# Performance work log

Measured on AMD Instinct MI355X. Metric: run time of the kernel, lower is better.

Reference implementation:

```python
import jax, jax.numpy as jnp
import numpy as np

HIDDEN_DIM = 64
MEMORY_SLOTS = 4
SEQ_LEN = 24
VOCAB_SIZE = 64
B = 65536


def setup_inputs() -> dict:
    key = jax.random.key(0)
    ks = jax.random.split(key, 16)
    s = 0.05
    inp = {
        "seqs": jax.random.randint(ks[0], (B, SEQ_LEN), 0, VOCAB_SIZE + 2),
        "query_tok": jax.random.randint(ks[1], (B,), 0, VOCAB_SIZE + 2),
        # embedding table [VOCAB+2, H]
        "embed": jax.random.normal(ks[2], (VOCAB_SIZE + 2, HIDDEN_DIM), jnp.float32) * s,
        # joint_net: Linear(H + S*H -> H), ReLU, Linear(H -> H), ReLU  (weights stored [in, out])
        "W1": jax.random.normal(ks[3], (HIDDEN_DIM + MEMORY_SLOTS * HIDDEN_DIM, HIDDEN_DIM), jnp.float32) * s,
        "b1": jax.random.normal(ks[4], (HIDDEN_DIM,), jnp.float32) * s,
        "W2": jax.random.normal(ks[5], (HIDDEN_DIM, HIDDEN_DIM), jnp.float32) * s,
        "b2": jax.random.normal(ks[6], (HIDDEN_DIM,), jnp.float32) * s,
        # write_head: Linear(H -> H)
        "Ww": jax.random.normal(ks[7], (HIDDEN_DIM, HIDDEN_DIM), jnp.float32) * s,
        "bw": jax.random.normal(ks[8], (HIDDEN_DIM,), jnp.float32) * s,
        # evict_head: Linear(H -> MEMORY_SLOTS)
        "We": jax.random.normal(ks[9], (HIDDEN_DIM, MEMORY_SLOTS), jnp.float32) * s,
        "be": jax.random.normal(ks[10], (MEMORY_SLOTS,), jnp.float32) * s,
        # read_head: Linear(2H -> H), ReLU, Linear(H -> VOCAB)
        "Wr1": jax.random.normal(ks[11], (2 * HIDDEN_DIM, HIDDEN_DIM), jnp.float32) * s,
        "br1": jax.random.normal(ks[12], (HIDDEN_DIM,), jnp.float32) * s,
        "Wr2": jax.random.normal(ks[13], (HIDDEN_DIM, VOCAB_SIZE), jnp.float32) * s,
        "br2": jax.random.normal(ks[14], (VOCAB_SIZE,), jnp.float32) * s,
    }
    return inp


def reference(seqs, query_tok, embed, W1, b1, W2, b2, Ww, bw, We, be, Wr1, br1, Wr2, br2):
    # Token embeddings for the first SEQ_LEN-1 positions, scanned over time: [T, B, H]
    emb_seq = jnp.swapaxes(embed[seqs[:, : SEQ_LEN - 1]], 0, 1)

    def step(mem, emb_t):  # mem: [B, S, H], emb_t: [B, H]
        joint_in = jnp.concatenate([emb_t, mem.reshape(mem.shape[0], -1)], axis=-1)  # [B, H + S*H]
        h = jax.nn.relu(joint_in @ W1 + b1)
        h = jax.nn.relu(h @ W2 + b2)                      # [B, H]
        write_vec = h @ Ww + bw                           # [B, H]
        evict_logits = h @ We + be                        # [B, S]
        evict_idx = jnp.argmax(evict_logits, axis=-1)     # [B] hard, non-diff
        mask = jax.nn.one_hot(evict_idx, MEMORY_SLOTS, dtype=bool)[..., None]  # [B, S, 1]
        new_mem = jnp.where(mask, write_vec[:, None, :], mem)
        return new_mem, None

    mem0 = jnp.zeros((seqs.shape[0], MEMORY_SLOTS, HIDDEN_DIM), jnp.float32)
    mem, _ = jax.lax.scan(step, mem0, emb_seq)

    mem_summary = mem.mean(axis=1)                        # [B, H]
    q_emb = embed[query_tok]                              # [B, H]
    r = jnp.concatenate([q_emb, mem_summary], axis=-1)    # [B, 2H]
    logits = jax.nn.relu(r @ Wr1 + br1) @ Wr2 + br2       # [B, VOCAB]
    return logits
```

## Files before the change

kernel.cpp:

```cpp
#include <hip/hip_runtime.h>

#define H       64
#define NSLOT   4
#define NSTEP   23
#define NB      65536
#define NV      66
#define SEQL    24
#define LPE     8
#define TPB     512
#define EPB     128
#define ACTSTR  68
#define MROW    68
#define JL      48
#define MSSTR   (JL * MROW + 4)

#define OFF_EW1   0
#define OFF_EWR1  (NV * H)
#define OFF_M     (2 * NV * H)
#define OFF_PB    (OFF_M + NSLOT * H * H)
#define OFF_HL    (OFF_PB + NSLOT * H)

__global__ __launch_bounds__(256) void k_setup_tables(
    const float* __restrict__ embed, const float* __restrict__ W1, const float* __restrict__ b1,
    const float* __restrict__ Wr1, const float* __restrict__ br1, float* __restrict__ ws)
{
    int idx = blockIdx.x * 256 + threadIdx.x;
    if (idx >= NV * H) return;
    int t = idx >> 6, k = idx & 63;
    float a1 = b1[k], a2 = br1[k];
    for (int j = 0; j < H; ++j) {
        float e = embed[t * H + j];
        a1 = fmaf(e, W1[j * H + k], a1);
        a2 = fmaf(e, Wr1[j * H + k], a2);
    }
    ws[OFF_EW1 + idx]  = a1;
    ws[OFF_EWR1 + idx] = a2;
}

__global__ __launch_bounds__(256) void k_setup_fuse(
    const float* __restrict__ W1, const float* __restrict__ Ww, const float* __restrict__ bw,
    float* __restrict__ ws)
{
    int idx = blockIdx.x * 256 + threadIdx.x;
    if (idx < NSLOT * H * H) {
        int s = idx >> 12, j = (idx >> 6) & 63, k = idx & 63;
        const float* w1s = W1 + (size_t)(H + s * H) * H;
        float acc = 0.f;
        for (int p = 0; p < H; ++p)
            acc = fmaf(Ww[j * H + p], w1s[p * H + k], acc);
        ws[OFF_M + idx] = acc;
    } else if (idx < NSLOT * H * H + NSLOT * H) {
        int r = idx - NSLOT * H * H;
        int s = r >> 6, k = r & 63;
        const float* w1s = W1 + (size_t)(H + s * H) * H;
        float acc = 0.f;
        for (int p = 0; p < H; ++p)
            acc = fmaf(bw[p], w1s[p * H + k], acc);
        ws[OFF_PB + r] = acc;
    }
}

#define FMA8V(w0, w1, a, ACC) do {                                          \
    ACC[0]=fmaf((a),w0.x,ACC[0]); ACC[1]=fmaf((a),w0.y,ACC[1]);            \
    ACC[2]=fmaf((a),w0.z,ACC[2]); ACC[3]=fmaf((a),w0.w,ACC[3]);            \
    ACC[4]=fmaf((a),w1.x,ACC[4]); ACC[5]=fmaf((a),w1.y,ACC[5]);            \
    ACC[6]=fmaf((a),w1.z,ACC[6]); ACC[7]=fmaf((a),w1.w,ACC[7]);            \
} while (0)

#define LOAD8(ptr, A) do {                                                  \
    const float4* _b = (const float4*)(ptr);                                \
    float4 _b0 = _b[0], _b1 = _b[1];                                        \
    A[0]=_b0.x; A[1]=_b0.y; A[2]=_b0.z; A[3]=_b0.w;                        \
    A[4]=_b1.x; A[5]=_b1.y; A[6]=_b1.z; A[7]=_b1.w;                        \
} while (0)

#define STORE8(rowptr, A) do {                                              \
    float4* _d = (float4*)(rowptr);                                         \
    _d[0] = make_float4(A[0], A[1], A[2], A[3]);                            \
    _d[1] = make_float4(A[4], A[5], A[6], A[7]);                            \
} while (0)

__global__ __launch_bounds__(TPB, 1) void k_main(
    const float* __restrict__ W2, const float* __restrict__ b2,
    const float* __restrict__ Ww, const float* __restrict__ bw,
    const float* __restrict__ We, const float* __restrict__ be,
    const float* __restrict__ Wr1, const float* __restrict__ Wr2, const float* __restrict__ br2,
    const int* __restrict__ qtok, const int* __restrict__ seqs,
    const float* __restrict__ ws, float* hl, float* __restrict__ out)
{
    __shared__ float sM[NSLOT * MSSTR];
    __shared__ float sAct[EPB * ACTSTR];
    __shared__ float sPb[NSLOT * 68];
    __shared__ float sWeS[8 * 36];

    const int tid  = threadIdx.x;
    const int m    = tid & (LPE - 1);
    const int g    = tid >> 3;
    const int eA   = g;
    const int eB   = g + 64;
    const int gidA = blockIdx.x * EPB + eA;
    const int gidB = blockIdx.x * EPB + eB;
    const int k0   = m * 8;

    if (tid < 256) {
        int s = tid >> 6, j = tid & 63;
        if (j < JL) {
            const float4* src = (const float4*)(ws + OFF_M + (size_t)(s * H + j) * H);
            float4* dst = (float4*)(sM + s * MSSTR + j * MROW);
#pragma unroll
            for (int k = 0; k < 16; ++k) dst[k] = src[k];
        }
    }
    if (tid >= 256 && tid < 512) {
        int r = tid - 256;
        int s = r >> 6, k = r & 63;
        sPb[s * 68 + k] = ws[OFF_PB + s * H + k];
    }
    if (tid < 256) {
        int mm = tid >> 5, rem = tid & 31;
        sWeS[mm * 36 + rem] = We[tid];
    }
    __syncthreads();

    const float* embW1b  = ws + OFF_EW1;
    const float* embWr1b = ws + OFF_EWR1;
    const float* Mg      = ws + OFF_M;
    float* hlA = hl + (size_t)gidA * (NSLOT * H) + k0;
    float* hlB = hl + (size_t)gidB * (NSLOT * H) + k0;

    float pA0[8], pA1[8], pA2[8], pA3[8], cA[8];
    float pB0[8], pB1[8], pB2[8], pB3[8], cB[8];
#pragma unroll
    for (int i = 0; i < 8; ++i) {
        pA0[i]=0.f; pA1[i]=0.f; pA2[i]=0.f; pA3[i]=0.f; cA[i]=0.f;
        pB0[i]=0.f; pB1[i]=0.f; pB2[i]=0.f; pB3[i]=0.f; cB[i]=0.f;
    }
    int maskA = 0, maskB = 0;

    float b2r[8];
    LOAD8(b2 + k0, b2r);
    const float4 be4 = *(const float4*)be;

    int tokA = seqs[gidA * SEQL];
    int tokB = seqs[gidB * SEQL];

    float accA[8], accB[8];
    float* rowA = sAct + eA * ACTSTR;
    float* rowB = sAct + eB * ACTSTR;

#pragma unroll 1
    for (int t = 0; t < NSTEP; ++t) {
        int tokAn = seqs[gidA * SEQL + t + 1];
        int tokBn = seqs[gidB * SEQL + t + 1];

        {
            float hA[8], hB[8];
            LOAD8(embW1b + tokA * H + k0, hA);
            LOAD8(embW1b + tokB * H + k0, hB);
#pragma unroll
            for (int i = 0; i < 8; ++i) {
                hA[i] = fmaxf(hA[i] + cA[i], 0.f);
                hB[i] = fmaxf(hB[i] + cB[i], 0.f);
            }
            STORE8(rowA + k0, hA);
            STORE8(rowB + k0, hB);
        }

#pragma unroll
        for (int i = 0; i < 8; ++i) { accA[i] = b2r[i]; accB[i] = b2r[i]; }
#pragma unroll 4
        for (int jq = 0; jq < 16; ++jq) {
            float4 a4 = *(const float4*)(rowA + jq * 4);
            float4 b4 = *(const float4*)(rowB + jq * 4);
            float aAv[4] = {a4.x, a4.y, a4.z, a4.w};
            float aBv[4] = {b4.x, b4.y, b4.z, b4.w};
#pragma unroll
            for (int jj = 0; jj < 4; ++jj) {
                const float4* w = (const float4*)(W2 + (jq * 4 + jj) * H + k0);
                float4 w0 = w[0], w1 = w[1];
                FMA8V(w0, w1, aAv[jj], accA);
                FMA8V(w0, w1, aBv[jj], accB);
            }
        }
        float h2A[8], h2B[8];
#pragma unroll
        for (int i = 0; i < 8; ++i) {
            h2A[i] = fmaxf(accA[i], 0.f);
            h2B[i] = fmaxf(accB[i], 0.f);
        }
        STORE8(rowA + k0, h2A);
        STORE8(rowB + k0, h2B);

        float lA0 = 0.f, lA1 = 0.f, lA2 = 0.f, lA3 = 0.f;
        float lB0 = 0.f, lB1 = 0.f, lB2 = 0.f, lB3 = 0.f;
        {
            const float* wsl = sWeS + m * 36;
#pragma unroll
            for (int i = 0; i < 8; ++i) {
                float4 we4 = *(const float4*)(wsl + i * 4);
                lA0 = fmaf(h2A[i], we4.x, lA0); lA1 = fmaf(h2A[i], we4.y, lA1);
                lA2 = fmaf(h2A[i], we4.z, lA2); lA3 = fmaf(h2A[i], we4.w, lA3);
                lB0 = fmaf(h2B[i], we4.x, lB0); lB1 = fmaf(h2B[i], we4.y, lB1);
                lB2 = fmaf(h2B[i], we4.z, lB2); lB3 = fmaf(h2B[i], we4.w, lB3);
            }
        }
#pragma unroll
        for (int d = 1; d <= 4; d <<= 1) {
            lA0 += __shfl_xor(lA0, d); lA1 += __shfl_xor(lA1, d);
            lA2 += __shfl_xor(lA2, d); lA3 += __shfl_xor(lA3, d);
            lB0 += __shfl_xor(lB0, d); lB1 += __shfl_xor(lB1, d);
            lB2 += __shfl_xor(lB2, d); lB3 += __shfl_xor(lB3, d);
        }
        lA0 += be4.x; lA1 += be4.y; lA2 += be4.z; lA3 += be4.w;
        lB0 += be4.x; lB1 += be4.y; lB2 += be4.z; lB3 += be4.w;

        int eSA = 0; float bstA = lA0;
        if (lA1 > bstA) { bstA = lA1; eSA = 1; }
        if (lA2 > bstA) { bstA = lA2; eSA = 2; }
        if (lA3 > bstA) { bstA = lA3; eSA = 3; }
        int eSB = 0; float bstB = lB0;
        if (lB1 > bstB) { bstB = lB1; eSB = 1; }
        if (lB2 > bstB) { bstB = lB2; eSB = 2; }
        if (lB3 > bstB) { bstB = lB3; eSB = 3; }

        bool a0 = (eSA == 0), a1 = (eSA == 1), a2 = (eSA == 2), a3 = (eSA == 3);
        bool b0 = (eSB == 0), b1 = (eSB == 1), b2_ = (eSB == 2), b3 = (eSB == 3);

        STORE8(hlA + eSA * H, h2A);
        STORE8(hlB + eSB * H, h2B);
        maskA |= (1 << eSA);
        maskB |= (1 << eSB);

        LOAD8(sPb + eSA * 68 + k0, accA);
        LOAD8(sPb + eSB * 68 + k0, accB);
        const float* lMA = sM + eSA * MSSTR + k0;
        const float* lMB = sM + eSB * MSSTR + k0;
#pragma unroll 4
        for (int jq = 0; jq < JL / 4; ++jq) {
            float4 a4 = *(const float4*)(rowA + jq * 4);
            float4 b4 = *(const float4*)(rowB + jq * 4);
            float dAv[4] = {a4.x, a4.y, a4.z, a4.w};
            float dBv[4] = {b4.x, b4.y, b4.z, b4.w};
#pragma unroll
            for (int jj = 0; jj < 4; ++jj) {
                int j = jq * 4 + jj;
                const float4* wa = (const float4*)(lMA + j * MROW);
                const float4* wb = (const float4*)(lMB + j * MROW);
                float4 wa0 = wa[0], wa1 = wa[1];
                float4 wb0 = wb[0], wb1 = wb[1];
                FMA8V(wa0, wa1, dAv[jj], accA);
                FMA8V(wb0, wb1, dBv[jj], accB);
            }
        }
        {
            const float* gMA = Mg + (size_t)(eSA * H + JL) * H + k0;
            const float* gMB = Mg + (size_t)(eSB * H + JL) * H + k0;
#pragma unroll 2
            for (int jq = JL / 4; jq < 16; ++jq) {
                float4 a4 = *(const float4*)(rowA + jq * 4);
                float4 b4 = *(const float4*)(rowB + jq * 4);
                float dAv[4] = {a4.x, a4.y, a4.z, a4.w};
                float dBv[4] = {b4.x, b4.y, b4.z, b4.w};
#pragma unroll
                for (int jj = 0; jj < 4; ++jj) {
                    int jr = (jq * 4 + jj) - JL;
                    const float4* wa = (const float4*)(gMA + jr * H);
                    const float4* wb = (const float4*)(gMB + jr * H);
                    float4 wa0 = wa[0], wa1 = wa[1];
                    float4 wb0 = wb[0], wb1 = wb[1];
                    FMA8V(wa0, wa1, dAv[jj], accA);
                    FMA8V(wb0, wb1, dBv[jj], accB);
                }
            }
        }

#pragma unroll
        for (int i = 0; i < 8; ++i) {
            float pvA = accA[i], pvB = accB[i];
            float oldA = a0 ? pA0[i] : a1 ? pA1[i] : a2 ? pA2[i] : pA3[i];
            float oldB = b0 ? pB0[i] : b1 ? pB1[i] : b2_ ? pB2[i] : pB3[i];
            cA[i] += pvA - oldA;
            cB[i] += pvB - oldB;
            pA0[i] = a0 ? pvA : pA0[i];  pA1[i] = a1 ? pvA : pA1[i];
            pA2[i] = a2 ? pvA : pA2[i];  pA3[i] = a3 ? pvA : pA3[i];
            pB0[i] = b0 ? pvB : pB0[i];  pB1[i] = b1 ? pvB : pB1[i];
            pB2[i] = b2_ ? pvB : pB2[i]; pB3[i] = b3 ? pvB : pB3[i];
        }

        tokA = tokAn; tokB = tokBn;
    }

    __threadfence();
    {
        float hsA[8] = {0,0,0,0,0,0,0,0}, hsB[8] = {0,0,0,0,0,0,0,0};
#pragma unroll
        for (int s = 0; s < NSLOT; ++s) {
            float vA[8], vB[8];
            LOAD8(hlA + s * H, vA);
            LOAD8(hlB + s * H, vB);
            float fA = ((maskA >> s) & 1) ? 1.f : 0.f;
            float fB = ((maskB >> s) & 1) ? 1.f : 0.f;
#pragma unroll
            for (int i = 0; i < 8; ++i) {
                hsA[i] = fmaf(fA, vA[i], hsA[i]);
                hsB[i] = fmaf(fB, vB[i], hsB[i]);
            }
        }
        STORE8(rowA + k0, hsA);
        STORE8(rowB + k0, hsB);
    }

    {
        float bwr[8];
        LOAD8(bw + k0, bwr);
        float cntA = (float)__popc(maskA), cntB = (float)__popc(maskB);
#pragma unroll
        for (int i = 0; i < 8; ++i) { accA[i] = cntA * bwr[i]; accB[i] = cntB * bwr[i]; }
    }
#pragma unroll 4
    for (int jq = 0; jq < 16; ++jq) {
        float4 a4 = *(const float4*)(rowA + jq * 4);
        float4 b4 = *(const float4*)(rowB + jq * 4);
        float aAv[4] = {a4.x, a4.y, a4.z, a4.w};
        float aBv[4] = {b4.x, b4.y, b4.z, b4.w};
#pragma unroll
        for (int jj = 0; jj < 4; ++jj) {
            const float4* w = (const float4*)(Ww + (jq * 4 + jj) * H + k0);
            float4 w0 = w[0], w1 = w[1];
            FMA8V(w0, w1, aAv[jj], accA);
            FMA8V(w0, w1, aBv[jj], accB);
        }
    }
    {
        float msA[8], msB[8];
#pragma unroll
        for (int i = 0; i < 8; ++i) {
            msA[i] = accA[i] * 0.25f;
            msB[i] = accB[i] * 0.25f;
        }
        STORE8(rowA + k0, msA);
        STORE8(rowB + k0, msB);
    }

    int qA = qtok[gidA], qB = qtok[gidB];
    LOAD8(embWr1b + qA * H + k0, accA);
    LOAD8(embWr1b + qB * H + k0, accB);
#pragma unroll 4
    for (int jq = 0; jq < 16; ++jq) {
        float4 a4 = *(const float4*)(rowA + jq * 4);
        float4 b4 = *(const float4*)(rowB + jq * 4);
        float aAv[4] = {a4.x, a4.y, a4.z, a4.w};
        float aBv[4] = {b4.x, b4.y, b4.z, b4.w};
#pragma unroll
        for (int jj = 0; jj < 4; ++jj) {
            const float4* w = (const float4*)(Wr1 + (H + jq * 4 + jj) * H + k0);
            float4 w0 = w[0], w1 = w[1];
            FMA8V(w0, w1, aAv[jj], accA);
            FMA8V(w0, w1, aBv[jj], accB);
        }
    }
    {
        float rA[8], rB[8];
#pragma unroll
        for (int i = 0; i < 8; ++i) {
            rA[i] = fmaxf(accA[i], 0.f);
            rB[i] = fmaxf(accB[i], 0.f);
        }
        STORE8(rowA + k0, rA);
        STORE8(rowB + k0, rB);
    }

    LOAD8(br2 + k0, accA);
#pragma unroll
    for (int i = 0; i < 8; ++i) accB[i] = accA[i];
#pragma unroll 4
    for (int jq = 0; jq < 16; ++jq) {
        float4 a4 = *(const float4*)(rowA + jq * 4);
        float4 b4 = *(const float4*)(rowB + jq * 4);
        float aAv[4] = {a4.x, a4.y, a4.z, a4.w};
        float aBv[4] = {b4.x, b4.y, b4.z, b4.w};
#pragma unroll
        for (int jj = 0; jj < 4; ++jj) {
            const float4* w = (const float4*)(Wr2 + (jq * 4 + jj) * H + k0);
            float4 w0 = w[0], w1 = w[1];
            FMA8V(w0, w1, aAv[jj], accA);
            FMA8V(w0, w1, aBv[jj], accB);
        }
    }

    float4* oA = (float4*)(out + (size_t)gidA * H + k0);
    oA[0] = make_float4(accA[0], accA[1], accA[2], accA[3]);
    oA[1] = make_float4(accA[4], accA[5], accA[6], accA[7]);
    float4* oB = (float4*)(out + (size_t)gidB * H + k0);
    oB[0] = make_float4(accB[0], accB[1], accB[2], accB[3]);
    oB[1] = make_float4(accB[4], accB[5], accB[6], accB[7]);
}

extern "C" void kernel_launch(void* const* d_in, const int* in_sizes, int n_in,
                              void* d_out, int out_size, void* d_ws, size_t ws_size,
                              hipStream_t stream)
{
    const int*   seqs  = (const int*)d_in[0];
    const int*   qtok  = (const int*)d_in[1];
    const float* embed = (const float*)d_in[2];
    const float* W1    = (const float*)d_in[3];
    const float* b1    = (const float*)d_in[4];
    const float* W2    = (const float*)d_in[5];
    const float* b2    = (const float*)d_in[6];
    const float* Ww    = (const float*)d_in[7];
    const float* bw    = (const float*)d_in[8];
    const float* We    = (const float*)d_in[9];
    const float* be    = (const float*)d_in[10];
    const float* Wr1   = (const float*)d_in[11];
    const float* br1   = (const float*)d_in[12];
    const float* Wr2   = (const float*)d_in[13];
    const float* br2   = (const float*)d_in[14];
    float* out = (float*)d_out;
    float* ws  = (float*)d_ws;

    hipLaunchKernelGGL(k_setup_tables, dim3((NV * H + 255) / 256), dim3(256), 0, stream,
                       embed, W1, b1, Wr1, br1, ws);
    hipLaunchKernelGGL(k_setup_fuse, dim3((NSLOT * H * H + NSLOT * H + 255) / 256), dim3(256),
                       0, stream, W1, Ww, bw, ws);
    hipLaunchKernelGGL(k_main, dim3(NB / EPB), dim3(TPB), 0, stream,
                       W2, b2, Ww, bw, We, be, Wr1, Wr2, br2, qtok, seqs,
                       ws, ws + OFF_HL, out);
}
```

Before: 811.2 us.

## Stagger the two per-thread sequences and interleave W2 and memory-projection matmuls

The two batch elements each thread handles now run half a step apart. Each half-step fuses one element's memory-projection matmul (via the selected slot's M matrix) with the other element's W2 matmul, so the argmax dependency chain of one overlaps the arithmetic of the other. A prologue and epilogue handle the offset, and the final step's unused projection matmul is skipped. The cost is that W2 rows are no longer shared between the two elements, so W2 weights are loaded twice as often per step.

```diff
diff --git a/kernel.cpp b/kernel.cpp
--- a/kernel.cpp
+++ b/kernel.cpp
@@ -13,6 +13,7 @@
 #define MROW    68
 #define JL      48
 #define MSSTR   (JL * MROW + 4)
+
 
 #define OFF_EW1   0
 #define OFF_EWR1  (NV * H)
@@ -80,6 +81,98 @@
     _d[1] = make_float4(A[4], A[5], A[6], A[7]);                            \
 } while (0)
 
+__device__ __forceinline__ void merged_pv_w2(
+    const float* rowPV, const float* rowW2,
+    const float* lM, const float* gM, const float* W2k,
+    float accPV[8], float accW2[8])
+{
+#pragma unroll 4
+    for (int jq = 0; jq < JL / 4; ++jq) {
+        float4 p4 = *(const float4*)(rowPV + jq * 4);
+        float4 w4 = *(const float4*)(rowW2 + jq * 4);
+        float pv_[4] = {p4.x, p4.y, p4.z, p4.w};
+        float wv_[4] = {w4.x, w4.y, w4.z, w4.w};
+#pragma unroll
+        for (int jj = 0; jj < 4; ++jj) {
+            int j = jq * 4 + jj;
+            const float4* wm = (const float4*)(lM + j * MROW);
+            float4 m0 = wm[0], m1 = wm[1];
+            const float4* wp = (const float4*)(W2k + j * H);
+            float4 w0 = wp[0], w1 = wp[1];
+            FMA8V(m0, m1, pv_[jj], accPV);
+            FMA8V(w0, w1, wv_[jj], accW2);
+        }
+    }
+#pragma unroll 2
+    for (int jq = JL / 4; jq < 16; ++jq) {
+        float4 p4 = *(const float4*)(rowPV + jq * 4);
+        float4 w4 = *(const float4*)(rowW2 + jq * 4);
+        float pv_[4] = {p4.x, p4.y, p4.z, p4.w};
+        float wv_[4] = {w4.x, w4.y, w4.z, w4.w};
+#pragma unroll
+        for (int jj = 0; jj < 4; ++jj) {
+            int j = jq * 4 + jj;
+            const float4* wm = (const float4*)(gM + (j - JL) * H);
+            float4 m0 = wm[0], m1 = wm[1];
+            const float4* wp = (const float4*)(W2k + j * H);
+            float4 w0 = wp[0], w1 = wp[1];
+            FMA8V(m0, m1, pv_[jj], accPV);
+            FMA8V(w0, w1, wv_[jj], accW2);
+        }
+    }
+}
+
+__device__ __forceinline__ void w2_only(const float* rowW2, const float* W2k, float accW2[8])
+{
+#pragma unroll 4
+    for (int jq = 0; jq < 16; ++jq) {
+        float4 w4 = *(const float4*)(rowW2 + jq * 4);
+        float wv_[4] = {w4.x, w4.y, w4.z, w4.w};
+#pragma unroll
+        for (int jj = 0; jj < 4; ++jj) {
+            const float4* wp = (const float4*)(W2k + (jq * 4 + jj) * H);
+            float4 w0 = wp[0], w1 = wp[1];
+            FMA8V(w0, w1, wv_[jj], accW2);
+        }
+    }
+}
+
+__device__ __forceinline__ int evict_sel(const float h2[8], const float* wsl, float4 be4)
+{
+    float l0 = 0.f, l1 = 0.f, l2 = 0.f, l3 = 0.f;
+#pragma unroll
+    for (int i = 0; i < 8; ++i) {
+        float4 we4 = *(const float4*)(wsl + i * 4);
+        l0 = fmaf(h2[i], we4.x, l0); l1 = fmaf(h2[i], we4.y, l1);
+        l2 = fmaf(h2[i], we4.z, l2); l3 = fmaf(h2[i], we4.w, l3);
+    }
+#pragma unroll
+    for (int d = 1; d <= 4; d <<= 1) {
+        l0 += __shfl_xor(l0, d); l1 += __shfl_xor(l1, d);
+        l2 += __shfl_xor(l2, d); l3 += __shfl_xor(l3, d);
+    }
+    l0 += be4.x; l1 += be4.y; l2 += be4.z; l3 += be4.w;
+    int e = 0; float b = l0;
+    if (l1 > b) { b = l1; e = 1; }
+    if (l2 > b) { b = l2; e = 2; }
+    if (l3 > b) { b = l3; e = 3; }
+    return e;
+}
+
+__device__ __forceinline__ void upd_contrib(int eS, const float pv[8], float c[8],
+                                            float p0[8], float p1[8], float p2[8], float p3[8])
+{
+    bool f0 = (eS == 0), f1 = (eS == 1), f2 = (eS == 2), f3 = (eS == 3);
+#pragma unroll
+    for (int i = 0; i < 8; ++i) {
+        float v = pv[i];
+        float old = f0 ? p0[i] : f1 ? p1[i] : f2 ? p2[i] : p3[i];
+        c[i] += v - old;
+        p0[i] = f0 ? v : p0[i]; p1[i] = f1 ? v : p1[i];
+        p2[i] = f2 ? v : p2[i]; p3[i] = f3 ? v : p3[i];
+    }
+}
+
 __global__ __launch_bounds__(TPB, 1) void k_main(
     const float* __restrict__ W2, const float* __restrict__ b2,
     const float* __restrict__ Ww, const float* __restrict__ bw,
@@ -125,6 +218,7 @@
     const float* embW1b  = ws + OFF_EW1;
     const float* embWr1b = ws + OFF_EWR1;
     const float* Mg      = ws + OFF_M;
+    const float* W2k     = W2 + k0;
     float* hlA = hl + (size_t)gidA * (NSLOT * H) + k0;
     float* hlB = hl + (size_t)gidB * (NSLOT * H) + k0;
 
@@ -144,153 +238,108 @@
     int tokA = seqs[gidA * SEQL];
     int tokB = seqs[gidB * SEQL];
 
-    float accA[8], accB[8];
     float* rowA = sAct + eA * ACTSTR;
     float* rowB = sAct + eB * ACTSTR;
 
+    int eSA;
+
+    {
+        float hA[8];
+        LOAD8(embW1b + tokA * H + k0, hA);
+#pragma unroll
+        for (int i = 0; i < 8; ++i) hA[i] = fmaxf(hA[i] + cA[i], 0.f);
+        STORE8(rowA + k0, hA);
+        float accWA[8];
+#pragma unroll
+        for (int i = 0; i < 8; ++i) accWA[i] = b2r[i];
+        w2_only(rowA, W2k, accWA);
+        float h2A[8];
+#pragma unroll
+        for (int i = 0; i < 8; ++i) h2A[i] = fmaxf(accWA[i], 0.f);
+        STORE8(rowA + k0, h2A);
+        eSA = evict_sel(h2A, sWeS + m * 36, be4);
+        STORE8(hlA + eSA * H, h2A);
+        maskA |= 1 << eSA;
+    }
+
 #pragma unroll 1
-    for (int t = 0; t < NSTEP; ++t) {
-        int tokAn = seqs[gidA * SEQL + t + 1];
-        int tokBn = seqs[gidB * SEQL + t + 1];
-
+    for (int t = 0; t < NSTEP - 1; ++t) {
         {
-            float hA[8], hB[8];
-            LOAD8(embW1b + tokA * H + k0, hA);
+            float hB[8];
             LOAD8(embW1b + tokB * H + k0, hB);
 #pragma unroll
-            for (int i = 0; i < 8; ++i) {
-                hA[i] = fmaxf(hA[i] + cA[i], 0.f);
-                hB[i] = fmaxf(hB[i] + cB[i], 0.f);
+            for (int i = 0; i < 8; ++i) hB[i] = fmaxf(hB[i] + cB[i], 0.f);
+            STORE8(rowB + k0, hB);
+        }
+        {
+            float accPA[8];
+            LOAD8(sPb + eSA * 68 + k0, accPA);
+            float accWB[8];
+#pragma unroll
+            for (int i = 0; i < 8; ++i) accWB[i] = b2r[i];
+            merged_pv_w2(rowA, rowB,
+                         sM + eSA * MSSTR + k0,
+                         Mg + (size_t)(eSA * H + JL) * H + k0,
+                         W2k, accPA, accWB);
+            float h2B[8];
+#pragma unroll
+            for (int i = 0; i < 8; ++i) h2B[i] = fmaxf(accWB[i], 0.f);
+            STORE8(rowB + k0, h2B);
+            int eSB = evict_sel(h2B, sWeS + m * 36, be4);
+            STORE8(hlB + eSB * H, h2B);
+            maskB |= 1 << eSB;
+            upd_contrib(eSA, accPA, cA, pA0, pA1, pA2, pA3);
+
+            {
+                int tokA1 = seqs[gidA * SEQL + t + 1];
+                float hA[8];
+                LOAD8(embW1b + tokA1 * H + k0, hA);
+#pragma unroll
+                for (int i = 0; i < 8; ++i) hA[i] = fmaxf(hA[i] + cA[i], 0.f);
+                STORE8(rowA + k0, hA);
             }
-            STORE8(rowA + k0, hA);
-            STORE8(rowB + k0, hB);
-        }
-
-#pragma unroll
-        for (int i = 0; i < 8; ++i) { accA[i] = b2r[i]; accB[i] = b2r[i]; }
-#pragma unroll 4
-        for (int jq = 0; jq < 16; ++jq) {
-            float4 a4 = *(const float4*)(rowA + jq * 4);
-            float4 b4 = *(const float4*)(rowB + jq * 4);
-            float aAv[4] = {a4.x, a4.y, a4.z, a4.w};
-            float aBv[4] = {b4.x, b4.y, b4.z, b4.w};
-#pragma unroll
-            for (int jj = 0; jj < 4; ++jj) {
-                const float4* w = (const float4*)(W2 + (jq * 4 + jj) * H + k0);
-                float4 w0 = w[0], w1 = w[1];
-                FMA8V(w0, w1, aAv[jj], accA);
-                FMA8V(w0, w1, aBv[jj], accB);
-            }
-        }
-        float h2A[8], h2B[8];
-#pragma unroll
-        for (int i = 0; i < 8; ++i) {
-            h2A[i] = fmaxf(accA[i], 0.f);
-            h2B[i] = fmaxf(accB[i], 0.f);
-        }
-        STORE8(rowA + k0, h2A);
+            float accPB[8];
+            LOAD8(sPb + eSB * 68 + k0, accPB);
+            float accWA[8];
+#pragma unroll
+            for (int i = 0; i < 8; ++i) accWA[i] = b2r[i];
+            merged_pv_w2(rowB, rowA,
+                         sM + eSB * MSSTR + k0,
+                         Mg + (size_t)(eSB * H + JL) * H + k0,
+                         W2k, accPB, accWA);
+            float h2A[8];
+#pragma unroll
+            for (int i = 0; i < 8; ++i) h2A[i] = fmaxf(accWA[i], 0.f);
+            STORE8(rowA + k0, h2A);
+            eSA = evict_sel(h2A, sWeS + m * 36, be4);
+            STORE8(hlA + eSA * H, h2A);
+            maskA |= 1 << eSA;
+            upd_contrib(eSB, accPB, cB, pB0, pB1, pB2, pB3);
+        }
+        tokB = seqs[gidB * SEQL + t + 1];
+    }
+
+    {
+        float hB[8];
+        LOAD8(embW1b + tokB * H + k0, hB);
+#pragma unroll
+        for (int i = 0; i < 8; ++i) hB[i] = fmaxf(hB[i] + cB[i], 0.f);
+        STORE8(rowB + k0, hB);
+        float accWB[8];
+#pragma unroll
+        for (int i = 0; i < 8; ++i) accWB[i] = b2r[i];
+        w2_only(rowB, W2k, accWB);
+        float h2B[8];
+#pragma unroll
+        for (int i = 0; i < 8; ++i) h2B[i] = fmaxf(accWB[i], 0.f);
         STORE8(rowB + k0, h2B);
-
-        float lA0 = 0.f, lA1 = 0.f, lA2 = 0.f, lA3 = 0.f;
-        float lB0 = 0.f, lB1 = 0.f, lB2 = 0.f, lB3 = 0.f;
-        {
-            const float* wsl = sWeS + m * 36;
-#pragma unroll
-            for (int i = 0; i < 8; ++i) {
-                float4 we4 = *(const float4*)(wsl + i * 4);
-                lA0 = fmaf(h2A[i], we4.x, lA0); lA1 = fmaf(h2A[i], we4.y, lA1);
-                lA2 = fmaf(h2A[i], we4.z, lA2); lA3 = fmaf(h2A[i], we4.w, lA3);
-                lB0 = fmaf(h2B[i], we4.x, lB0); lB1 = fmaf(h2B[i], we4.y, lB1);
-                lB2 = fmaf(h2B[i], we4.z, lB2); lB3 = fmaf(h2B[i], we4.w, lB3);
-            }
-        }
-#pragma unroll
-        for (int d = 1; d <= 4; d <<= 1) {
-            lA0 += __shfl_xor(lA0, d); lA1 += __shfl_xor(lA1, d);
-            lA2 += __shfl_xor(lA2, d); lA3 += __shfl_xor(lA3, d);
-            lB0 += __shfl_xor(lB0, d); lB1 += __shfl_xor(lB1, d);
-            lB2 += __shfl_xor(lB2, d); lB3 += __shfl_xor(lB3, d);
-        }
-        lA0 += be4.x; lA1 += be4.y; lA2 += be4.z; lA3 += be4.w;
-        lB0 += be4.x; lB1 += be4.y; lB2 += be4.z; lB3 += be4.w;
-
-        int eSA = 0; float bstA = lA0;
-        if (lA1 > bstA) { bstA = lA1; eSA = 1; }
-        if (lA2 > bstA) { bstA = lA2; eSA = 2; }
-        if (lA3 > bstA) { bstA = lA3; eSA = 3; }
-        int eSB = 0; float bstB = lB0;
-        if (lB1 > bstB) { bstB = lB1; eSB = 1; }
-        if (lB2 > bstB) { bstB = lB2; eSB = 2; }
-        if (lB3 > bstB) { bstB = lB3; eSB = 3; }
-
-        bool a0 = (eSA == 0), a1 = (eSA == 1), a2 = (eSA == 2), a3 = (eSA == 3);
-        bool b0 = (eSB == 0), b1 = (eSB == 1), b2_ = (eSB == 2), b3 = (eSB == 3);
-
-        STORE8(hlA + eSA * H, h2A);
+        int eSB = evict_sel(h2B, sWeS + m * 36, be4);
         STORE8(hlB + eSB * H, h2B);
-        maskA |= (1 << eSA);
-        maskB |= (1 << eSB);
-
-        LOAD8(sPb + eSA * 68 + k0, accA);
-        LOAD8(sPb + eSB * 68 + k0, accB);
-        const float* lMA = sM + eSA * MSSTR + k0;
-        const float* lMB = sM + eSB * MSSTR + k0;
-#pragma unroll 4
-        for (int jq = 0; jq < JL / 4; ++jq) {
-            float4 a4 = *(const float4*)(rowA + jq * 4);
-            float4 b4 = *(const float4*)(rowB + jq * 4);
-            float dAv[4] = {a4.x, a4.y, a4.z, a4.w};
-            float dBv[4] = {b4.x, b4.y, b4.z, b4.w};
-#pragma unroll
-            for (int jj = 0; jj < 4; ++jj) {
-                int j = jq * 4 + jj;
-                const float4* wa = (const float4*)(lMA + j * MROW);
-                const float4* wb = (const float4*)(lMB + j * MROW);
-                float4 wa0 = wa[0], wa1 = wa[1];
-                float4 wb0 = wb[0], wb1 = wb[1];
-                FMA8V(wa0, wa1, dAv[jj], accA);
-                FMA8V(wb0, wb1, dBv[jj], accB);
-            }
-        }
-        {
-            const float* gMA = Mg + (size_t)(eSA * H + JL) * H + k0;
-            const float* gMB = Mg + (size_t)(eSB * H + JL) * H + k0;
-#pragma unroll 2
-            for (int jq = JL / 4; jq < 16; ++jq) {
-                float4 a4 = *(const float4*)(rowA + jq * 4);
-                float4 b4 = *(const float4*)(rowB + jq * 4);
-                float dAv[4] = {a4.x, a4.y, a4.z, a4.w};
-                float dBv[4] = {b4.x, b4.y, b4.z, b4.w};
-#pragma unroll
-                for (int jj = 0; jj < 4; ++jj) {
-                    int jr = (jq * 4 + jj) - JL;
-                    const float4* wa = (const float4*)(gMA + jr * H);
-                    const float4* wb = (const float4*)(gMB + jr * H);
-                    float4 wa0 = wa[0], wa1 = wa[1];
-                    float4 wb0 = wb[0], wb1 = wb[1];
-                    FMA8V(wa0, wa1, dAv[jj], accA);
-                    FMA8V(wb0, wb1, dBv[jj], accB);
-                }
-            }
-        }
-
-#pragma unroll
-        for (int i = 0; i < 8; ++i) {
-            float pvA = accA[i], pvB = accB[i];
-            float oldA = a0 ? pA0[i] : a1 ? pA1[i] : a2 ? pA2[i] : pA3[i];
-            float oldB = b0 ? pB0[i] : b1 ? pB1[i] : b2_ ? pB2[i] : pB3[i];
-            cA[i] += pvA - oldA;
-            cB[i] += pvB - oldB;
-            pA0[i] = a0 ? pvA : pA0[i];  pA1[i] = a1 ? pvA : pA1[i];
-            pA2[i] = a2 ? pvA : pA2[i];  pA3[i] = a3 ? pvA : pA3[i];
-            pB0[i] = b0 ? pvB : pB0[i];  pB1[i] = b1 ? pvB : pB1[i];
-            pB2[i] = b2_ ? pvB : pB2[i]; pB3[i] = b3 ? pvB : pB3[i];
-        }
-
-        tokA = tokAn; tokB = tokBn;
+        maskB |= 1 << eSB;
     }
 
     __threadfence();
+    float accA[8], accB[8];
     {
         float hsA[8] = {0,0,0,0,0,0,0,0}, hsB[8] = {0,0,0,0,0,0,0,0};
 #pragma unroll
```

Measured after the change: 1.113 ms. 1.37x slower.

## Keep full slot projection matrix in LDS and peel the last recurrence step

Applied to the files above, without the earlier changes.

The per-slot projection matrices are now staged into shared memory in full instead of the first 48 rows, which removes the global-memory tail loop from the inner product. The final time step is peeled out of the loop so it skips the slot-projection matvec and the running-sum update, whose results are never used after the last write. Staging all rows raises LDS use per block, which may lower occupancy.

```diff
diff --git a/kernel.cpp b/kernel.cpp
--- a/kernel.cpp
+++ b/kernel.cpp
@@ -11,7 +11,7 @@
 #define EPB     128
 #define ACTSTR  68
 #define MROW    68
-#define JL      48
+#define JL      64
 #define MSSTR   (JL * MROW + 4)
 
 #define OFF_EW1   0
@@ -104,12 +104,10 @@
 
     if (tid < 256) {
         int s = tid >> 6, j = tid & 63;
-        if (j < JL) {
-            const float4* src = (const float4*)(ws + OFF_M + (size_t)(s * H + j) * H);
-            float4* dst = (float4*)(sM + s * MSSTR + j * MROW);
-#pragma unroll
-            for (int k = 0; k < 16; ++k) dst[k] = src[k];
-        }
+        const float4* src = (const float4*)(ws + OFF_M + (size_t)(s * H + j) * H);
+        float4* dst = (float4*)(sM + s * MSSTR + j * MROW);
+#pragma unroll
+        for (int k = 0; k < 16; ++k) dst[k] = src[k];
     }
     if (tid >= 256 && tid < 512) {
         int r = tid - 256;
@@ -124,7 +122,6 @@
 
     const float* embW1b  = ws + OFF_EW1;
     const float* embWr1b = ws + OFF_EWR1;
-    const float* Mg      = ws + OFF_M;
     float* hlA = hl + (size_t)gidA * (NSLOT * H) + k0;
     float* hlB = hl + (size_t)gidB * (NSLOT * H) + k0;
 
@@ -149,7 +146,7 @@
     float* rowB = sAct + eB * ACTSTR;
 
 #pragma unroll 1
-    for (int t = 0; t < NSTEP; ++t) {
+    for (int t = 0; t < NSTEP - 1; ++t) {
         int tokAn = seqs[gidA * SEQL + t + 1];
         int tokBn = seqs[gidB * SEQL + t + 1];
 
@@ -236,7 +233,7 @@
         const float* lMA = sM + eSA * MSSTR + k0;
         const float* lMB = sM + eSB * MSSTR + k0;
 #pragma unroll 4
-        for (int jq = 0; jq < JL / 4; ++jq) {
+        for (int jq = 0; jq < 16; ++jq) {
             float4 a4 = *(const float4*)(rowA + jq * 4);
             float4 b4 = *(const float4*)(rowB + jq * 4);
             float dAv[4] = {a4.x, a4.y, a4.z, a4.w};
@@ -250,27 +247,6 @@
                 float4 wb0 = wb[0], wb1 = wb[1];
                 FMA8V(wa0, wa1, dAv[jj], accA);
                 FMA8V(wb0, wb1, dBv[jj], accB);
-            }
-        }
-        {
-            const float* gMA = Mg + (size_t)(eSA * H + JL) * H + k0;
-            const float* gMB = Mg + (size_t)(eSB * H + JL) * H + k0;
-#pragma unroll 2
-            for (int jq = JL / 4; jq < 16; ++jq) {
-                float4 a4 = *(const float4*)(rowA + jq * 4);
-                float4 b4 = *(const float4*)(rowB + jq * 4);
-                float dAv[4] = {a4.x, a4.y, a4.z, a4.w};
-                float dBv[4] = {b4.x, b4.y, b4.z, b4.w};
-#pragma unroll
-                for (int jj = 0; jj < 4; ++jj) {
-                    int jr = (jq * 4 + jj) - JL;
-                    const float4* wa = (const float4*)(gMA + jr * H);
-                    const float4* wb = (const float4*)(gMB + jr * H);
-                    float4 wa0 = wa[0], wa1 = wa[1];
-                    float4 wb0 = wb[0], wb1 = wb[1];
-                    FMA8V(wa0, wa1, dAv[jj], accA);
-                    FMA8V(wb0, wb1, dBv[jj], accB);
-                }
             }
         }
 
@@ -288,6 +264,79 @@
         }
 
         tokA = tokAn; tokB = tokBn;
+    }
+
+    {
+        float hA[8], hB[8];
+        LOAD8(embW1b + tokA * H + k0, hA);
+        LOAD8(embW1b + tokB * H + k0, hB);
+#pragma unroll
+        for (int i = 0; i < 8; ++i) {
+            hA[i] = fmaxf(hA[i] + cA[i], 0.f);
+            hB[i] = fmaxf(hB[i] + cB[i], 0.f);
+        }
+        STORE8(rowA + k0, hA);
+        STORE8(rowB + k0, hB);
+
+#pragma unroll
+        for (int i = 0; i < 8; ++i) { accA[i] = b2r[i]; accB[i] = b2r[i]; }
+#pragma unroll 4
+        for (int jq = 0; jq < 16; ++jq) {
+            float4 a4 = *(const float4*)(rowA + jq * 4);
+            float4 b4 = *(const float4*)(rowB + jq * 4);
+            float aAv[4] = {a4.x, a4.y, a4.z, a4.w};
+            float aBv[4] = {b4.x, b4.y, b4.z, b4.w};
+#pragma unroll
+            for (int jj = 0; jj < 4; ++jj) {
+                const float4* w = (const float4*)(W2 + (jq * 4 + jj) * H + k0);
+                float4 w0 = w[0], w1 = w[1];
+                FMA8V(w0, w1, aAv[jj], accA);
+                FMA8V(w0, w1, aBv[jj], accB);
+            }
+        }
+        float h2A[8], h2B[8];
+#pragma unroll
+        for (int i = 0; i < 8; ++i) {
+            h2A[i] = fmaxf(accA[i], 0.f);
+            h2B[i] = fmaxf(accB[i], 0.f);
+        }
+
+        float lA0 = 0.f, lA1 = 0.f, lA2 = 0.f, lA3 = 0.f;
+        float lB0 = 0.f, lB1 = 0.f, lB2 = 0.f, lB3 = 0.f;
+        {
+            const float* wsl = sWeS + m * 36;
+#pragma unroll
+            for (int i = 0; i < 8; ++i) {
+                float4 we4 = *(const float4*)(wsl + i * 4);
+                lA0 = fmaf(h2A[i], we4.x, lA0); lA1 = fmaf(h2A[i], we4.y, lA1);
+                lA2 = fmaf(h2A[i], we4.z, lA2); lA3 = fmaf(h2A[i], we4.w, lA3);
+                lB0 = fmaf(h2B[i], we4.x, lB0); lB1 = fmaf(h2B[i], we4.y, lB1);
+                lB2 = fmaf(h2B[i], we4.z, lB2); lB3 = fmaf(h2B[i], we4.w, lB3);
+            }
+        }
+#pragma unroll
+        for (int d = 1; d <= 4; d <<= 1) {
+            lA0 += __shfl_xor(lA0, d); lA1 += __shfl_xor(lA1, d);
+            lA2 += __shfl_xor(lA2, d); lA3 += __shfl_xor(lA3, d);
+            lB0 += __shfl_xor(lB0, d); lB1 += __shfl_xor(lB1, d);
+            lB2 += __shfl_xor(lB2, d); lB3 += __shfl_xor(lB3, d);
+        }
+        lA0 += be4.x; lA1 += be4.y; lA2 += be4.z; lA3 += be4.w;
+        lB0 += be4.x; lB1 += be4.y; lB2 += be4.z; lB3 += be4.w;
+
+        int eSA = 0; float bstA = lA0;
+        if (lA1 > bstA) { bstA = lA1; eSA = 1; }
+        if (lA2 > bstA) { bstA = lA2; eSA = 2; }
+        if (lA3 > bstA) { bstA = lA3; eSA = 3; }
+        int eSB = 0; float bstB = lB0;
+        if (lB1 > bstB) { bstB = lB1; eSB = 1; }
+        if (lB2 > bstB) { bstB = lB2; eSB = 2; }
+        if (lB3 > bstB) { bstB = lB3; eSB = 3; }
+
+        STORE8(hlA + eSA * H, h2A);
+        STORE8(hlB + eSB * H, h2B);
+        maskA |= (1 << eSA);
+        maskB |= (1 << eSB);
     }
 
     __threadfence();
```

After: 851.2 us. 1.05x slower.
